# Kernel optimization log

Hardware: AMD Instinct MI355X
Metric: run time of the kernel (lower is better)

Reference implementation:

```python
import jax, jax.numpy as jnp
import numpy as np


def _ln(x, g, b, eps=1e-5):
    m = x.mean(-1, keepdims=True)
    v = ((x - m) ** 2).mean(-1, keepdims=True)
    return (x - m) * jax.lax.rsqrt(v + eps) * g + b


def setup_inputs() -> dict:
    key = jax.random.key(0)
    ks = jax.random.split(key, 12)
    B, S, I, H, E, P, O, EM = 32, 512, 64, 512, 8, 96, 64, 512
    D = S * I
    r = lambda k, shape, s=0.02: jax.random.normal(k, shape, jnp.float32) * s
    z = lambda *shape: jnp.zeros(shape, jnp.float32)
    o = lambda *shape: jnp.ones(shape, jnp.float32)
    return dict(
        x=jax.random.normal(ks[0], (B, S, I), jnp.float32),
        gW1=r(ks[1], (D, EM)), gb1=z(EM), gln1_g=o(EM), gln1_b=z(EM),
        gW2=r(ks[2], (EM, EM)), gb2=z(EM), gln2_g=o(EM), gln2_b=z(EM),
        gW3=r(ks[3], (EM, 128)), gb3=z(128),
        protos=jax.random.normal(ks[4], (E, 128), jnp.float32) * 0.01,
        temp=jnp.ones((), jnp.float32),
        eW1=r(ks[5], (E, I, H)), eb1=z(E, H),
        eW2=r(ks[6], (E, H, H)), eb2=z(E, H),
        fW1=r(ks[7], (H, H)), fb1=z(H), fln_g=o(H), fln_b=z(H),
        fW2=r(ks[8], (H, H)), fb2=z(H),
        ln_g=o(H), ln_b=z(H),
        pW1=r(ks[9], (H, H // 2)), pb1=z(H // 2), pln_g=o(H // 2), pln_b=z(H // 2),
        pW2=r(ks[10], (H // 2, P * O)), pb2=z(P * O),
        on_g=o(O), on_b=z(O),
    )


def reference(x, gW1, gb1, gln1_g, gln1_b, gW2, gb2, gln2_g, gln2_b, gW3, gb3,
              protos, temp, eW1, eb1, eW2, eb2,
              fW1, fb1, fln_g, fln_b, fW2, fb2, ln_g, ln_b,
              pW1, pb1, pln_g, pln_b, pW2, pb2, on_g, on_b):
    B, S, I = x.shape
    O = on_g.shape[0]
    P = pW2.shape[1] // O
    # 1) flow latent mapping (identity fallback path of the original code)
    x_flat = x.reshape(B, S * I)
    z_latent = x_flat
    # 2) gating encoder -> 128-d embedding (dropout = identity in eval)
    h = jax.nn.relu(_ln(z_latent @ gW1 + gb1, gln1_g, gln1_b))
    h = jax.nn.relu(_ln(h @ gW2 + gb2, gln2_g, gln2_b))
    emb = h @ gW3 + gb3  # [B, 128]
    # 3) routing: euclidean cdist to prototypes, temperature-scaled softmax
    d2 = jnp.sum((emb[:, None, :] - protos[None, :, :]) ** 2, axis=-1)
    dist = jnp.sqrt(jnp.maximum(d2, 1e-12))  # [B, E]
    t = jnp.clip(temp, 0.1, 5.0)
    w = jax.nn.softmax(-dist / t, axis=-1)  # [B, E]
    # 4) experts: per-expert FFN on raw input, all experts batched
    he = jax.nn.relu(jnp.einsum('bsi,eih->besh', x, eW1) + eb1[None, :, None, :])
    eo = jnp.einsum('besh,eho->beso', he, eW2) + eb2[None, :, None, :]  # [B,E,S,H]
    # 5) routing-weighted combine + fusion + prediction head
    fused = jnp.einsum('besh,be->bsh', eo, w)
    f = jax.nn.relu(_ln(fused @ fW1 + fb1, fln_g, fln_b)) @ fW2 + fb2
    f = _ln(f, ln_g, ln_b)
    last = f[:, -1, :]  # [B, H]
    p = jax.nn.relu(_ln(last @ pW1 + pb1, pln_g, pln_b)) @ pW2 + pb2
    p = p.reshape(B, P, O)
    return _ln(p, on_g, on_b)
```

## Files before the change

kernel.cpp:

```cpp
#include <hip/hip_runtime.h>
#include <math.h>

#define DIMK 32768

__device__ __forceinline__ void fma4(float4& a, float s, const float4 w) {
  a.x += s * w.x; a.y += s * w.y; a.z += s * w.z; a.w += s * w.w;
}

__device__ __forceinline__ float block_sum(float v, float* red, int n) {
  int t = threadIdx.x;
  red[t] = v;
  __syncthreads();
  for (int s = n >> 1; s > 0; s >>= 1) {
    if (t < s) red[t] += red[t + s];
    __syncthreads();
  }
  float r = red[0];
  __syncthreads();
  return r;
}

__global__ __launch_bounds__(256) void gemm1(const float* __restrict__ x,
                                             const float* __restrict__ gW1,
                                             float* __restrict__ part) {
  const int mt = blockIdx.x, ks = blockIdx.y;
  const int m0 = mt * 128, k0 = ks * 256;
  const int t = threadIdx.x;
  __shared__ float As[32 * 260];
  __shared__ float Ws[64 * 128];

  for (int i = t; i < 2048; i += 256) {
    int b = i >> 6, q = i & 63;
    *(float4*)&As[b * 260 + q * 4] = *(const float4*)(x + (size_t)b * DIMK + k0 + q * 4);
  }
  const float* Wp = gW1 + (size_t)k0 * 512 + m0;
  float4 wreg[8];
#pragma unroll
  for (int j = 0; j < 8; ++j) {
    int i = t + j * 256, r = i >> 5, q = i & 31;
    wreg[j] = *(const float4*)(Wp + (size_t)r * 512 + q * 4);
  }

  const int mf = t & 31, bg = t >> 5;
  const int b0 = bg * 4;
  float4 acc[4];
#pragma unroll
  for (int j = 0; j < 4; ++j) acc[j] = make_float4(0.f, 0.f, 0.f, 0.f);
  const float* a0 = &As[b0 * 260];

  for (int s = 0; s < 4; ++s) {
    __syncthreads();
#pragma unroll
    for (int j = 0; j < 8; ++j) {
      int i = t + j * 256, r = i >> 5, q = i & 31;
      *(float4*)&Ws[r * 128 + q * 4] = wreg[j];
    }
    __syncthreads();
    if (s < 3) {
      const float* Wn = Wp + (size_t)(s + 1) * 64 * 512;
#pragma unroll
      for (int j = 0; j < 8; ++j) {
        int i = t + j * 256, r = i >> 5, q = i & 31;
        wreg[j] = *(const float4*)(Wn + (size_t)r * 512 + q * 4);
      }
    }
    const float* ab = a0 + s * 64;
#pragma unroll 8
    for (int k = 0; k < 64; ++k) {
      float4 wv = *(const float4*)&Ws[k * 128 + mf * 4];
      float av0 = ab[k], av1 = ab[260 + k], av2 = ab[520 + k], av3 = ab[780 + k];
      fma4(acc[0], av0, wv);
      fma4(acc[1], av1, wv);
      fma4(acc[2], av2, wv);
      fma4(acc[3], av3, wv);
    }
  }

  float* op = part + ((size_t)ks * 32 + b0) * 512 + m0 + mf * 4;
#pragma unroll
  for (int j = 0; j < 4; ++j) *(float4*)(op + (size_t)j * 512) = acc[j];
}

__global__ __launch_bounds__(512) void gred_ln(const float* __restrict__ part,
                                               const float* __restrict__ gb1,
                                               const float* __restrict__ g, const float* __restrict__ bt,
                                               float* __restrict__ h1) {
  const int b = blockIdx.x, t = threadIdx.x;
  __shared__ float red[512];
  float a = gb1[t];
  const float* pp0 = part + (size_t)b * 512 + t;
#pragma unroll 8
  for (int ks = 0; ks < 128; ++ks) a += pp0[(size_t)ks * 16384];
  float mean = block_sum(a, red, 512) * (1.f / 512.f);
  float d = a - mean;
  float var = block_sum(d * d, red, 512) * (1.f / 512.f);
  h1[b * 512 + t] = fmaxf(d * rsqrtf(var + 1e-5f) * g[t] + bt[t], 0.f);
}

template <int KC>
__global__ __launch_bounds__(256) void gemm_tile(const float* __restrict__ A,
                                                 const float* __restrict__ W,
                                                 float* __restrict__ outp,
                                                 int M, int aRow,
                                                 size_t aStrideE, size_t wStrideE) {
  const int mt = blockIdx.x, kq = blockIdx.y, e = blockIdx.z, NE = gridDim.z;
  const int m0 = mt * 64, k0 = kq * KC;
  const int t = threadIdx.x;
  __shared__ float Ws[KC * 64];
  __shared__ float As[32 * (KC + 4)];
  const float* Wp = W + (size_t)e * wStrideE + (size_t)k0 * M + m0;
  for (int i = t; i < KC * 16; i += 256) {
    int r = i >> 4, q = i & 15;
    *(float4*)&Ws[r * 64 + q * 4] = *(const float4*)(Wp + (size_t)r * M + q * 4);
  }
  const float* Ap = A + (size_t)e * aStrideE + k0;
  for (int i = t; i < 32 * (KC / 4); i += 256) {
    int b = i / (KC / 4), q = i % (KC / 4);
    *(float4*)&As[b * (KC + 4) + q * 4] = *(const float4*)(Ap + (size_t)b * aRow + q * 4);
  }
  __syncthreads();
  const int mf = t & 15, bg = t >> 4;
  const int b0 = bg * 2;
  float4 acc0 = make_float4(0.f, 0.f, 0.f, 0.f), acc1 = acc0;
  const float* a0 = &As[b0 * (KC + 4)];
  const float* a1 = &As[(b0 + 1) * (KC + 4)];
#pragma unroll 8
  for (int k = 0; k < KC; ++k) {
    float4 wv = *(const float4*)&Ws[k * 64 + mf * 4];
    fma4(acc0, a0[k], wv);
    fma4(acc1, a1[k], wv);
  }
  float* op = outp + ((size_t)(kq * NE + e) * 32 + b0) * M + m0 + mf * 4;
  *(float4*)op = acc0;
  *(float4*)(op + M) = acc1;
}

__global__ void red_ln(const float* __restrict__ zp, const float* __restrict__ bias,
                       const float* __restrict__ g, const float* __restrict__ bt,
                       float* __restrict__ outp, int M, int nq, int relu) {
  const int b = blockIdx.x, t = threadIdx.x;
  __shared__ float red[512];
  float a = bias[t];
#pragma unroll 4
  for (int kq = 0; kq < nq; ++kq) a += zp[((size_t)kq * 32 + b) * M + t];
  float fM = 1.f / (float)M;
  float mean = block_sum(a, red, M) * fM;
  float d = a - mean;
  float var = block_sum(d * d, red, M) * fM;
  float v = d * rsqrtf(var + 1e-5f) * g[t] + bt[t];
  outp[b * M + t] = relu ? fmaxf(v, 0.f) : v;
}

__global__ __launch_bounds__(128) void gate_k(const float* __restrict__ zp2,
                                              const float* __restrict__ gb3,
                                              const float* __restrict__ protos,
                                              const float* __restrict__ temp,
                                              float* __restrict__ wgt) {
  __shared__ float red[128];
  __shared__ float d2s[8];
  const int b = blockIdx.x, t = threadIdx.x;
  float a = gb3[t];
#pragma unroll 4
  for (int kq = 0; kq < 16; ++kq) a += zp2[((size_t)kq * 32 + b) * 128 + t];
  for (int e = 0; e < 8; ++e) {
    float dd = a - protos[e * 128 + t];
    float s = block_sum(dd * dd, red, 128);
    if (t == 0) d2s[e] = s;
  }
  __syncthreads();
  if (t == 0) {
    float tt = fminf(fmaxf(temp[0], 0.1f), 5.0f);
    float lg[8], mx = -1e30f;
#pragma unroll
    for (int e = 0; e < 8; ++e) {
      float dist = sqrtf(fmaxf(d2s[e], 1e-12f));
      lg[e] = -dist / tt;
      mx = fmaxf(mx, lg[e]);
    }
    float se = 0.f;
#pragma unroll
    for (int e = 0; e < 8; ++e) { lg[e] = expf(lg[e] - mx); se += lg[e]; }
#pragma unroll
    for (int e = 0; e < 8; ++e) wgt[b * 8 + e] = lg[e] / se;
  }
}

__global__ __launch_bounds__(256) void he_k(const float* __restrict__ x,
                                            const float* __restrict__ eW1,
                                            const float* __restrict__ eb1,
                                            float* __restrict__ he_all) {
  const int e = blockIdx.x, hs = blockIdx.y;
  const int t = threadIdx.x;
  __shared__ float xs[32 * 64];
  __shared__ float Ws[64 * 256];
  for (int i = t; i < 512; i += 256) {
    int b = i >> 4, q = i & 15;
    *(float4*)&xs[b * 64 + q * 4] = *(const float4*)(x + (size_t)b * DIMK + 32704 + q * 4);
  }
  const float* w1 = eW1 + (size_t)e * 64 * 512 + hs * 256;
  for (int i = t; i < 64 * 64; i += 256) {
    int k = i >> 6, q = i & 63;
    *(float4*)&Ws[k * 256 + q * 4] = *(const float4*)(w1 + (size_t)k * 512 + q * 4);
  }
  __syncthreads();
  float acc[32];
#pragma unroll
  for (int b = 0; b < 32; ++b) acc[b] = 0.f;
#pragma unroll 4
  for (int k = 0; k < 64; ++k) {
    float wk = Ws[k * 256 + t];
#pragma unroll
    for (int b = 0; b < 32; ++b) acc[b] += xs[b * 64 + k] * wk;
  }
  float bb = eb1[e * 512 + hs * 256 + t];
  for (int b = 0; b < 32; ++b)
    he_all[((size_t)e * 32 + b) * 512 + hs * 256 + t] = fmaxf(acc[b] + bb, 0.f);
}

__global__ __launch_bounds__(512) void ffuse(const float* __restrict__ epart,
                                             const float* __restrict__ eb2,
                                             const float* __restrict__ wgt,
                                             float* __restrict__ fused) {
  const int b = blockIdx.x, t = threadIdx.x;
  __shared__ float wl[8];
  if (t < 8) wl[t] = wgt[b * 8 + t];
  __syncthreads();
  float a = 0.f;
#pragma unroll
  for (int e = 0; e < 8; ++e) {
    float s = eb2[e * 512 + t];
#pragma unroll
    for (int kq = 0; kq < 8; ++kq)
      s += epart[(((size_t)kq * 8 + e) * 32 + b) * 512 + t];
    a += wl[e] * s;
  }
  fused[b * 512 + t] = a;
}

__global__ __launch_bounds__(256) void fin_red(const float* __restrict__ fpart,
                                               const float* __restrict__ pb2,
                                               const float* __restrict__ ong,
                                               const float* __restrict__ onb,
                                               float* __restrict__ outp) {
  const int t = threadIdx.x;
  const int lane = t & 63, w = t >> 6;
  const int r = blockIdx.x * 4 + w;
  const int b = r / 96, pi = r % 96;
  const int m = pi * 64 + lane;
  float a = pb2[m];
#pragma unroll
  for (int kq = 0; kq < 8; ++kq) a += fpart[((size_t)kq * 32 + b) * 6144 + m];
  float s = a;
  s += __shfl_xor(s, 1); s += __shfl_xor(s, 2); s += __shfl_xor(s, 4);
  s += __shfl_xor(s, 8); s += __shfl_xor(s, 16); s += __shfl_xor(s, 32);
  float mean = s * (1.f / 64.f);
  float d = a - mean;
  float q = d * d;
  q += __shfl_xor(q, 1); q += __shfl_xor(q, 2); q += __shfl_xor(q, 4);
  q += __shfl_xor(q, 8); q += __shfl_xor(q, 16); q += __shfl_xor(q, 32);
  float rr = rsqrtf(q * (1.f / 64.f) + 1e-5f);
  outp[((size_t)b * 96 + pi) * 64 + lane] = d * rr * ong[lane] + onb[lane];
}

extern "C" void kernel_launch(void* const* d_in, const int* in_sizes, int n_in,
                              void* d_out, int out_size, void* d_ws, size_t ws_size,
                              hipStream_t stream) {
  (void)in_sizes; (void)n_in; (void)out_size; (void)ws_size;
  const float* x      = (const float*)d_in[0];
  const float* gW1    = (const float*)d_in[1];
  const float* gb1    = (const float*)d_in[2];
  const float* gln1_g = (const float*)d_in[3];
  const float* gln1_b = (const float*)d_in[4];
  const float* gW2    = (const float*)d_in[5];
  const float* gb2    = (const float*)d_in[6];
  const float* gln2_g = (const float*)d_in[7];
  const float* gln2_b = (const float*)d_in[8];
  const float* gW3    = (const float*)d_in[9];
  const float* gb3    = (const float*)d_in[10];
  const float* protos = (const float*)d_in[11];
  const float* temp   = (const float*)d_in[12];
  const float* eW1    = (const float*)d_in[13];
  const float* eb1    = (const float*)d_in[14];
  const float* eW2    = (const float*)d_in[15];
  const float* eb2    = (const float*)d_in[16];
  const float* fW1    = (const float*)d_in[17];
  const float* fb1    = (const float*)d_in[18];
  const float* fln_g  = (const float*)d_in[19];
  const float* fln_b  = (const float*)d_in[20];
  const float* fW2    = (const float*)d_in[21];
  const float* fb2    = (const float*)d_in[22];
  const float* ln_g   = (const float*)d_in[23];
  const float* ln_b   = (const float*)d_in[24];
  const float* pW1    = (const float*)d_in[25];
  const float* pb1    = (const float*)d_in[26];
  const float* pln_g  = (const float*)d_in[27];
  const float* pln_b  = (const float*)d_in[28];
  const float* pW2    = (const float*)d_in[29];
  const float* pb2    = (const float*)d_in[30];
  const float* on_g   = (const float*)d_in[31];
  const float* on_b   = (const float*)d_in[32];
  float* out = (float*)d_out;

  float* ws     = (float*)d_ws;
  float* part   = ws;
  float* epart  = ws;
  float* he_all = ws + 1048576;
  float* fpart  = ws;
  float* h1     = ws + 2097152;
  float* h2     = h1 + 16384;
  float* zp     = h2 + 16384;
  float* zp2    = zp + 262144;
  float* wgt    = zp2 + 65536;
  float* fused  = wgt + 256;
  float* f1     = fused + 16384;
  float* lastv  = f1 + 16384;
  float* pp     = lastv + 16384;

  gemm1<<<dim3(4, 128), 256, 0, stream>>>(x, gW1, part);
  gred_ln<<<32, 512, 0, stream>>>(part, gb1, gln1_g, gln1_b, h1);
  gemm_tile<32><<<dim3(8, 16, 1), 256, 0, stream>>>(h1, gW2, zp, 512, 512, 0, 0);
  red_ln<<<32, 512, 0, stream>>>(zp, gb2, gln2_g, gln2_b, h2, 512, 16, 1);
  gemm_tile<32><<<dim3(2, 16, 1), 256, 0, stream>>>(h2, gW3, zp2, 128, 512, 0, 0);
  gate_k<<<32, 128, 0, stream>>>(zp2, gb3, protos, temp, wgt);

  he_k<<<dim3(8, 2), 256, 0, stream>>>(x, eW1, eb1, he_all);
  gemm_tile<64><<<dim3(8, 8, 8), 256, 0, stream>>>(he_all, eW2, epart, 512, 512,
                                                   (size_t)32 * 512, (size_t)512 * 512);
  ffuse<<<32, 512, 0, stream>>>(epart, eb2, wgt, fused);

  gemm_tile<32><<<dim3(8, 16, 1), 256, 0, stream>>>(fused, fW1, zp, 512, 512, 0, 0);
  red_ln<<<32, 512, 0, stream>>>(zp, fb1, fln_g, fln_b, f1, 512, 16, 1);
  gemm_tile<32><<<dim3(8, 16, 1), 256, 0, stream>>>(f1, fW2, zp, 512, 512, 0, 0);
  red_ln<<<32, 512, 0, stream>>>(zp, fb2, ln_g, ln_b, lastv, 512, 16, 0);
  gemm_tile<32><<<dim3(4, 16, 1), 256, 0, stream>>>(lastv, pW1, zp, 256, 512, 0, 0);
  red_ln<<<32, 256, 0, stream>>>(zp, pb1, pln_g, pln_b, pp, 256, 16, 1);

  gemm_tile<32><<<dim3(96, 8, 1), 256, 0, stream>>>(pp, pW2, fpart, 6144, 256, 0, 0);
  fin_red<<<768, 256, 0, stream>>>(fpart, pb2, on_g, on_b, out);
}
```

Measured before the change: 295.3 us.

## Collapse sixteen launches into four fused kernels with per-row MLP chains

Merges the gating GEMM with the expert first layer into one grid. The gating tail (LN, GEMM2, LN, GEMM3, routing softmax) now runs alongside the expert second-layer GEMM in a single launch. The fusion and prediction chain is done per batch row inside one block, and the final projection is fused with its LayerNorm. This removes many launches and the partial-sum round trips through global memory. In exchange, the per-row blocks read full weight matrices with low parallelism (32 blocks), which may leave the GPU underused on the serial MLP chain.

```diff
diff --git a/kernel.cpp b/kernel.cpp
--- a/kernel.cpp
+++ b/kernel.cpp
@@ -7,259 +7,324 @@
   a.x += s * w.x; a.y += s * w.y; a.z += s * w.z; a.w += s * w.w;
 }
 
-__device__ __forceinline__ float block_sum(float v, float* red, int n) {
-  int t = threadIdx.x;
-  red[t] = v;
-  __syncthreads();
-  for (int s = n >> 1; s > 0; s >>= 1) {
-    if (t < s) red[t] += red[t + s];
-    __syncthreads();
-  }
-  float r = red[0];
-  __syncthreads();
-  return r;
-}
-
-__global__ __launch_bounds__(256) void gemm1(const float* __restrict__ x,
-                                             const float* __restrict__ gW1,
-                                             float* __restrict__ part) {
-  const int mt = blockIdx.x, ks = blockIdx.y;
-  const int m0 = mt * 128, k0 = ks * 256;
+__device__ __forceinline__ float bsum8(float v, volatile float* r8) {
+  for (int o = 1; o < 64; o <<= 1) v += __shfl_xor(v, o);
+  const int w = threadIdx.x >> 6;
+  __syncthreads();
+  if ((threadIdx.x & 63) == 0) r8[w] = v;
+  __syncthreads();
+  float s = 0.f;
+#pragma unroll
+  for (int i = 0; i < 8; ++i) s += r8[i];
+  return s;
+}
+
+__global__ __launch_bounds__(256) void k1_gemm1_he(const float* __restrict__ x,
+                                                   const float* __restrict__ gW1,
+                                                   const float* __restrict__ eW1,
+                                                   const float* __restrict__ eb1,
+                                                   float* __restrict__ part,
+                                                   float* __restrict__ he_all) {
+  __shared__ __align__(16) float S[18432];
   const int t = threadIdx.x;
-  __shared__ float As[32 * 260];
-  __shared__ float Ws[64 * 128];
-
-  for (int i = t; i < 2048; i += 256) {
-    int b = i >> 6, q = i & 63;
-    *(float4*)&As[b * 260 + q * 4] = *(const float4*)(x + (size_t)b * DIMK + k0 + q * 4);
-  }
-  const float* Wp = gW1 + (size_t)k0 * 512 + m0;
-  float4 wreg[8];
-#pragma unroll
-  for (int j = 0; j < 8; ++j) {
-    int i = t + j * 256, r = i >> 5, q = i & 31;
-    wreg[j] = *(const float4*)(Wp + (size_t)r * 512 + q * 4);
-  }
-
-  const int mf = t & 31, bg = t >> 5;
-  const int b0 = bg * 4;
-  float4 acc[4];
-#pragma unroll
-  for (int j = 0; j < 4; ++j) acc[j] = make_float4(0.f, 0.f, 0.f, 0.f);
-  const float* a0 = &As[b0 * 260];
-
-  for (int s = 0; s < 4; ++s) {
-    __syncthreads();
+  if (blockIdx.x < 512) {
+    const int mt = blockIdx.x & 3, ks = blockIdx.x >> 2;
+    const int m0 = mt * 128, k0 = ks * 256;
+    float* As = S;
+    float* Ws = S + 8320;
+    for (int i = t; i < 2048; i += 256) {
+      int b = i >> 6, q = i & 63;
+      *(float4*)&As[b * 260 + q * 4] = *(const float4*)(x + (size_t)b * DIMK + k0 + q * 4);
+    }
+    const float* Wp = gW1 + (size_t)k0 * 512 + m0;
+    float4 wreg[8];
 #pragma unroll
     for (int j = 0; j < 8; ++j) {
       int i = t + j * 256, r = i >> 5, q = i & 31;
-      *(float4*)&Ws[r * 128 + q * 4] = wreg[j];
-    }
-    __syncthreads();
-    if (s < 3) {
-      const float* Wn = Wp + (size_t)(s + 1) * 64 * 512;
+      wreg[j] = *(const float4*)(Wp + (size_t)r * 512 + q * 4);
+    }
+    const int mf = t & 31, bg = t >> 5;
+    const int b0 = bg * 4;
+    float4 acc[4];
+#pragma unroll
+    for (int j = 0; j < 4; ++j) acc[j] = make_float4(0.f, 0.f, 0.f, 0.f);
+    const float* a0 = &As[b0 * 260];
+    for (int s = 0; s < 4; ++s) {
+      __syncthreads();
 #pragma unroll
       for (int j = 0; j < 8; ++j) {
         int i = t + j * 256, r = i >> 5, q = i & 31;
-        wreg[j] = *(const float4*)(Wn + (size_t)r * 512 + q * 4);
-      }
-    }
-    const float* ab = a0 + s * 64;
-#pragma unroll 8
+        *(float4*)&Ws[r * 128 + q * 4] = wreg[j];
+      }
+      __syncthreads();
+      if (s < 3) {
+        const float* Wn = Wp + (size_t)(s + 1) * 64 * 512;
+#pragma unroll
+        for (int j = 0; j < 8; ++j) {
+          int i = t + j * 256, r = i >> 5, q = i & 31;
+          wreg[j] = *(const float4*)(Wn + (size_t)r * 512 + q * 4);
+        }
+      }
+      const float* ab = a0 + s * 64;
+#pragma unroll 8
+      for (int k = 0; k < 64; ++k) {
+        float4 wv = *(const float4*)&Ws[k * 128 + mf * 4];
+        fma4(acc[0], ab[k], wv);
+        fma4(acc[1], ab[260 + k], wv);
+        fma4(acc[2], ab[520 + k], wv);
+        fma4(acc[3], ab[780 + k], wv);
+      }
+    }
+    float* op = part + ((size_t)ks * 32 + b0) * 512 + m0 + mf * 4;
+#pragma unroll
+    for (int j = 0; j < 4; ++j) *(float4*)(op + (size_t)j * 512) = acc[j];
+  } else {
+    const int v = blockIdx.x - 512;
+    const int e = v >> 1, hs = v & 1;
+    float* xs = S;
+    float* Ws = S + 2048;
+    for (int i = t; i < 512; i += 256) {
+      int b = i >> 4, q = i & 15;
+      *(float4*)&xs[b * 64 + q * 4] = *(const float4*)(x + (size_t)b * DIMK + 32704 + q * 4);
+    }
+    const float* w1 = eW1 + (size_t)e * 32768 + hs * 256;
+    for (int i = t; i < 4096; i += 256) {
+      int r = i >> 6, q = i & 63;
+      *(float4*)&Ws[r * 256 + q * 4] = *(const float4*)(w1 + (size_t)r * 512 + q * 4);
+    }
+    __syncthreads();
+    float acc[32];
+#pragma unroll
+    for (int b = 0; b < 32; ++b) acc[b] = 0.f;
+#pragma unroll 4
     for (int k = 0; k < 64; ++k) {
-      float4 wv = *(const float4*)&Ws[k * 128 + mf * 4];
-      float av0 = ab[k], av1 = ab[260 + k], av2 = ab[520 + k], av3 = ab[780 + k];
-      fma4(acc[0], av0, wv);
-      fma4(acc[1], av1, wv);
-      fma4(acc[2], av2, wv);
-      fma4(acc[3], av3, wv);
-    }
-  }
-
-  float* op = part + ((size_t)ks * 32 + b0) * 512 + m0 + mf * 4;
-#pragma unroll
-  for (int j = 0; j < 4; ++j) *(float4*)(op + (size_t)j * 512) = acc[j];
-}
-
-__global__ __launch_bounds__(512) void gred_ln(const float* __restrict__ part,
-                                               const float* __restrict__ gb1,
-                                               const float* __restrict__ g, const float* __restrict__ bt,
-                                               float* __restrict__ h1) {
+      float wk = Ws[k * 256 + t];
+#pragma unroll
+      for (int b = 0; b < 32; ++b) acc[b] += xs[b * 64 + k] * wk;
+    }
+    float bb = eb1[e * 512 + hs * 256 + t];
+    for (int b = 0; b < 32; ++b)
+      he_all[((size_t)e * 32 + b) * 512 + hs * 256 + t] = fmaxf(acc[b] + bb, 0.f);
+  }
+}
+
+__global__ __launch_bounds__(512) void k2_gtail_eg(const float* __restrict__ part,
+                                                   const float* __restrict__ gb1,
+                                                   const float* __restrict__ g1g, const float* __restrict__ g1b,
+                                                   const float* __restrict__ gW2, const float* __restrict__ gb2,
+                                                   const float* __restrict__ g2g, const float* __restrict__ g2b,
+                                                   const float* __restrict__ gW3, const float* __restrict__ gb3,
+                                                   const float* __restrict__ protos, const float* __restrict__ temp,
+                                                   const float* __restrict__ he_all, const float* __restrict__ eW2,
+                                                   float* __restrict__ wgt, float* __restrict__ eo) {
+  __shared__ __align__(16) float S[16512];
+  __shared__ float hb[512], h2b[512], embp[512], embs[128], d2s[8];
+  __shared__ float r8[8];
+  const int t = threadIdx.x;
+  if (blockIdx.x < 32) {
+    const int b = blockIdx.x;
+    float a = gb1[t];
+    const float* p0 = part + (size_t)b * 512 + t;
+#pragma unroll 8
+    for (int ks = 0; ks < 128; ++ks) a += p0[(size_t)ks * 16384];
+    float mean = bsum8(a, r8) * (1.f / 512.f);
+    float d = a - mean;
+    float var = bsum8(d * d, r8) * (1.f / 512.f);
+    hb[t] = fmaxf(d * rsqrtf(var + 1e-5f) * g1g[t] + g1b[t], 0.f);
+    __syncthreads();
+    float y = gb2[t];
+    {
+      const float* wp = gW2 + t;
+#pragma unroll 8
+      for (int k = 0; k < 512; ++k) y += hb[k] * wp[(size_t)k * 512];
+    }
+    mean = bsum8(y, r8) * (1.f / 512.f);
+    d = y - mean;
+    var = bsum8(d * d, r8) * (1.f / 512.f);
+    h2b[t] = fmaxf(d * rsqrtf(var + 1e-5f) * g2g[t] + g2b[t], 0.f);
+    __syncthreads();
+    {
+      const int kh = t >> 7, m = t & 127;
+      float c = 0.f;
+      const float* w3 = gW3 + m;
+#pragma unroll 8
+      for (int k = kh * 128; k < kh * 128 + 128; ++k) c += h2b[k] * w3[(size_t)k * 128];
+      embp[t] = c;
+    }
+    __syncthreads();
+    if (t < 128) embs[t] = gb3[t] + embp[t] + embp[128 + t] + embp[256 + t] + embp[384 + t];
+    __syncthreads();
+    {
+      const int e = t >> 6, l = t & 63;
+      float z0 = embs[l] - protos[e * 128 + l];
+      float z1 = embs[l + 64] - protos[e * 128 + 64 + l];
+      float q = z0 * z0 + z1 * z1;
+      for (int o = 1; o < 64; o <<= 1) q += __shfl_xor(q, o);
+      if (l == 0) d2s[e] = q;
+    }
+    __syncthreads();
+    if (t == 0) {
+      float tt = fminf(fmaxf(temp[0], 0.1f), 5.0f);
+      float lg[8], mx = -1e30f;
+#pragma unroll
+      for (int e = 0; e < 8; ++e) {
+        float dist = sqrtf(fmaxf(d2s[e], 1e-12f));
+        lg[e] = -dist / tt;
+        mx = fmaxf(mx, lg[e]);
+      }
+      float se = 0.f;
+#pragma unroll
+      for (int e = 0; e < 8; ++e) { lg[e] = expf(lg[e] - mx); se += lg[e]; }
+#pragma unroll
+      for (int e = 0; e < 8; ++e) wgt[b * 8 + e] = lg[e] / se;
+    }
+  } else {
+    const int v = blockIdx.x - 32;
+    const int e = v >> 3, mt = v & 7;
+    const int m0 = mt * 64;
+    float* As = S;
+    float* Ws = S + 8320;
+    const int mf = t & 15, bg = t >> 4;
+    float4 acc = make_float4(0.f, 0.f, 0.f, 0.f);
+    const float* Ae = he_all + (size_t)e * 16384;
+    const float* We = eW2 + (size_t)e * 262144 + m0;
+    for (int kh = 0; kh < 2; ++kh) {
+      __syncthreads();
+      for (int i = t; i < 2048; i += 512) {
+        int b = i >> 6, q = i & 63;
+        *(float4*)&As[b * 260 + q * 4] =
+            *(const float4*)(Ae + (size_t)b * 512 + kh * 256 + q * 4);
+      }
+      for (int sub = 0; sub < 2; ++sub) {
+        __syncthreads();
+        const float* wp = We + (size_t)(kh * 256 + sub * 128) * 512;
+        for (int i = t; i < 2048; i += 512) {
+          int r = i >> 4, q = i & 15;
+          *(float4*)&Ws[r * 64 + q * 4] = *(const float4*)(wp + (size_t)r * 512 + q * 4);
+        }
+        __syncthreads();
+        const float* ar = As + bg * 260 + sub * 128;
+#pragma unroll 8
+        for (int k = 0; k < 128; ++k)
+          fma4(acc, ar[k], *(const float4*)&Ws[k * 64 + mf * 4]);
+      }
+    }
+    *(float4*)(eo + ((size_t)e * 32 + bg) * 512 + m0 + mf * 4) = acc;
+  }
+}
+
+__global__ __launch_bounds__(512) void k3_fpath(const float* __restrict__ eo,
+                                                const float* __restrict__ eb2,
+                                                const float* __restrict__ wgt,
+                                                const float* __restrict__ fW1, const float* __restrict__ fb1,
+                                                const float* __restrict__ flg, const float* __restrict__ flb,
+                                                const float* __restrict__ fW2, const float* __restrict__ fb2,
+                                                const float* __restrict__ lng, const float* __restrict__ lnb,
+                                                const float* __restrict__ pW1, const float* __restrict__ pb1,
+                                                const float* __restrict__ plg, const float* __restrict__ plb,
+                                                float* __restrict__ pp) {
+  __shared__ float rowA[512], pl[512], r8[8], wl8[8];
   const int b = blockIdx.x, t = threadIdx.x;
-  __shared__ float red[512];
-  float a = gb1[t];
-  const float* pp0 = part + (size_t)b * 512 + t;
-#pragma unroll 8
-  for (int ks = 0; ks < 128; ++ks) a += pp0[(size_t)ks * 16384];
-  float mean = block_sum(a, red, 512) * (1.f / 512.f);
-  float d = a - mean;
-  float var = block_sum(d * d, red, 512) * (1.f / 512.f);
-  h1[b * 512 + t] = fmaxf(d * rsqrtf(var + 1e-5f) * g[t] + bt[t], 0.f);
-}
-
-template <int KC>
-__global__ __launch_bounds__(256) void gemm_tile(const float* __restrict__ A,
-                                                 const float* __restrict__ W,
-                                                 float* __restrict__ outp,
-                                                 int M, int aRow,
-                                                 size_t aStrideE, size_t wStrideE) {
-  const int mt = blockIdx.x, kq = blockIdx.y, e = blockIdx.z, NE = gridDim.z;
-  const int m0 = mt * 64, k0 = kq * KC;
-  const int t = threadIdx.x;
-  __shared__ float Ws[KC * 64];
-  __shared__ float As[32 * (KC + 4)];
-  const float* Wp = W + (size_t)e * wStrideE + (size_t)k0 * M + m0;
-  for (int i = t; i < KC * 16; i += 256) {
-    int r = i >> 4, q = i & 15;
-    *(float4*)&Ws[r * 64 + q * 4] = *(const float4*)(Wp + (size_t)r * M + q * 4);
-  }
-  const float* Ap = A + (size_t)e * aStrideE + k0;
-  for (int i = t; i < 32 * (KC / 4); i += 256) {
-    int b = i / (KC / 4), q = i % (KC / 4);
-    *(float4*)&As[b * (KC + 4) + q * 4] = *(const float4*)(Ap + (size_t)b * aRow + q * 4);
-  }
-  __syncthreads();
-  const int mf = t & 15, bg = t >> 4;
-  const int b0 = bg * 2;
-  float4 acc0 = make_float4(0.f, 0.f, 0.f, 0.f), acc1 = acc0;
-  const float* a0 = &As[b0 * (KC + 4)];
-  const float* a1 = &As[(b0 + 1) * (KC + 4)];
-#pragma unroll 8
-  for (int k = 0; k < KC; ++k) {
-    float4 wv = *(const float4*)&Ws[k * 64 + mf * 4];
-    fma4(acc0, a0[k], wv);
-    fma4(acc1, a1[k], wv);
-  }
-  float* op = outp + ((size_t)(kq * NE + e) * 32 + b0) * M + m0 + mf * 4;
-  *(float4*)op = acc0;
-  *(float4*)(op + M) = acc1;
-}
-
-__global__ void red_ln(const float* __restrict__ zp, const float* __restrict__ bias,
-                       const float* __restrict__ g, const float* __restrict__ bt,
-                       float* __restrict__ outp, int M, int nq, int relu) {
-  const int b = blockIdx.x, t = threadIdx.x;
-  __shared__ float red[512];
-  float a = bias[t];
-#pragma unroll 4
-  for (int kq = 0; kq < nq; ++kq) a += zp[((size_t)kq * 32 + b) * M + t];
-  float fM = 1.f / (float)M;
-  float mean = block_sum(a, red, M) * fM;
-  float d = a - mean;
-  float var = block_sum(d * d, red, M) * fM;
-  float v = d * rsqrtf(var + 1e-5f) * g[t] + bt[t];
-  outp[b * M + t] = relu ? fmaxf(v, 0.f) : v;
-}
-
-__global__ __launch_bounds__(128) void gate_k(const float* __restrict__ zp2,
-                                              const float* __restrict__ gb3,
-                                              const float* __restrict__ protos,
-                                              const float* __restrict__ temp,
-                                              float* __restrict__ wgt) {
-  __shared__ float red[128];
-  __shared__ float d2s[8];
-  const int b = blockIdx.x, t = threadIdx.x;
-  float a = gb3[t];
-#pragma unroll 4
-  for (int kq = 0; kq < 16; ++kq) a += zp2[((size_t)kq * 32 + b) * 128 + t];
-  for (int e = 0; e < 8; ++e) {
-    float dd = a - protos[e * 128 + t];
-    float s = block_sum(dd * dd, red, 128);
-    if (t == 0) d2s[e] = s;
-  }
-  __syncthreads();
-  if (t == 0) {
-    float tt = fminf(fmaxf(temp[0], 0.1f), 5.0f);
-    float lg[8], mx = -1e30f;
-#pragma unroll
-    for (int e = 0; e < 8; ++e) {
-      float dist = sqrtf(fmaxf(d2s[e], 1e-12f));
-      lg[e] = -dist / tt;
-      mx = fmaxf(mx, lg[e]);
-    }
-    float se = 0.f;
-#pragma unroll
-    for (int e = 0; e < 8; ++e) { lg[e] = expf(lg[e] - mx); se += lg[e]; }
-#pragma unroll
-    for (int e = 0; e < 8; ++e) wgt[b * 8 + e] = lg[e] / se;
-  }
-}
-
-__global__ __launch_bounds__(256) void he_k(const float* __restrict__ x,
-                                            const float* __restrict__ eW1,
-                                            const float* __restrict__ eb1,
-                                            float* __restrict__ he_all) {
-  const int e = blockIdx.x, hs = blockIdx.y;
-  const int t = threadIdx.x;
-  __shared__ float xs[32 * 64];
-  __shared__ float Ws[64 * 256];
-  for (int i = t; i < 512; i += 256) {
-    int b = i >> 4, q = i & 15;
-    *(float4*)&xs[b * 64 + q * 4] = *(const float4*)(x + (size_t)b * DIMK + 32704 + q * 4);
-  }
-  const float* w1 = eW1 + (size_t)e * 64 * 512 + hs * 256;
-  for (int i = t; i < 64 * 64; i += 256) {
-    int k = i >> 6, q = i & 63;
-    *(float4*)&Ws[k * 256 + q * 4] = *(const float4*)(w1 + (size_t)k * 512 + q * 4);
-  }
-  __syncthreads();
-  float acc[32];
-#pragma unroll
-  for (int b = 0; b < 32; ++b) acc[b] = 0.f;
-#pragma unroll 4
-  for (int k = 0; k < 64; ++k) {
-    float wk = Ws[k * 256 + t];
-#pragma unroll
-    for (int b = 0; b < 32; ++b) acc[b] += xs[b * 64 + k] * wk;
-  }
-  float bb = eb1[e * 512 + hs * 256 + t];
-  for (int b = 0; b < 32; ++b)
-    he_all[((size_t)e * 32 + b) * 512 + hs * 256 + t] = fmaxf(acc[b] + bb, 0.f);
-}
-
-__global__ __launch_bounds__(512) void ffuse(const float* __restrict__ epart,
-                                             const float* __restrict__ eb2,
-                                             const float* __restrict__ wgt,
-                                             float* __restrict__ fused) {
-  const int b = blockIdx.x, t = threadIdx.x;
-  __shared__ float wl[8];
-  if (t < 8) wl[t] = wgt[b * 8 + t];
-  __syncthreads();
-  float a = 0.f;
-#pragma unroll
-  for (int e = 0; e < 8; ++e) {
-    float s = eb2[e * 512 + t];
-#pragma unroll
-    for (int kq = 0; kq < 8; ++kq)
-      s += epart[(((size_t)kq * 8 + e) * 32 + b) * 512 + t];
-    a += wl[e] * s;
-  }
-  fused[b * 512 + t] = a;
-}
-
-__global__ __launch_bounds__(256) void fin_red(const float* __restrict__ fpart,
+  if (t < 8) wl8[t] = wgt[b * 8 + t];
+  __syncthreads();
+  {
+    float a = 0.f;
+#pragma unroll
+    for (int e = 0; e < 8; ++e)
+      a += wl8[e] * (eo[((size_t)e * 32 + b) * 512 + t] + eb2[e * 512 + t]);
+    rowA[t] = a;
+  }
+  __syncthreads();
+  {
+    float y = fb1[t];
+    const float* wp = fW1 + t;
+#pragma unroll 8
+    for (int k = 0; k < 512; ++k) y += rowA[k] * wp[(size_t)k * 512];
+    float mean = bsum8(y, r8) * (1.f / 512.f);
+    float d = y - mean;
+    float var = bsum8(d * d, r8) * (1.f / 512.f);
+    float v = d * rsqrtf(var + 1e-5f) * flg[t] + flb[t];
+    rowA[t] = fmaxf(v, 0.f);
+  }
+  __syncthreads();
+  {
+    float y = fb2[t];
+    const float* wp = fW2 + t;
+#pragma unroll 8
+    for (int k = 0; k < 512; ++k) y += rowA[k] * wp[(size_t)k * 512];
+    float mean = bsum8(y, r8) * (1.f / 512.f);
+    float d = y - mean;
+    float var = bsum8(d * d, r8) * (1.f / 512.f);
+    rowA[t] = d * rsqrtf(var + 1e-5f) * lng[t] + lnb[t];
+  }
+  __syncthreads();
+  {
+    const int half = t >> 8, j = t & 255;
+    float c = 0.f;
+    const float* wp = pW1 + j;
+#pragma unroll 8
+    for (int k = half * 256; k < half * 256 + 256; ++k) c += rowA[k] * wp[(size_t)k * 256];
+    pl[t] = c;
+  }
+  __syncthreads();
+  float val = 0.f;
+  if (t < 256) val = pl[t] + pl[256 + t] + pb1[t];
+  float mean = bsum8(t < 256 ? val : 0.f, r8) * (1.f / 256.f);
+  float d = val - mean;
+  float var = bsum8(t < 256 ? d * d : 0.f, r8) * (1.f / 256.f);
+  if (t < 256) {
+    float v = d * rsqrtf(var + 1e-5f) * plg[t] + plb[t];
+    pp[b * 256 + t] = fmaxf(v, 0.f);
+  }
+}
+
+__global__ __launch_bounds__(256) void k4_pfin(const float* __restrict__ pp,
+                                               const float* __restrict__ pW2,
                                                const float* __restrict__ pb2,
                                                const float* __restrict__ ong,
                                                const float* __restrict__ onb,
                                                float* __restrict__ outp) {
+  __shared__ __align__(16) float Ws[256 * 64];
+  __shared__ __align__(16) float As[8 * 260];
+  const int pi = blockIdx.x, bq = blockIdx.y;
   const int t = threadIdx.x;
-  const int lane = t & 63, w = t >> 6;
-  const int r = blockIdx.x * 4 + w;
-  const int b = r / 96, pi = r % 96;
-  const int m = pi * 64 + lane;
-  float a = pb2[m];
-#pragma unroll
-  for (int kq = 0; kq < 8; ++kq) a += fpart[((size_t)kq * 32 + b) * 6144 + m];
-  float s = a;
-  s += __shfl_xor(s, 1); s += __shfl_xor(s, 2); s += __shfl_xor(s, 4);
-  s += __shfl_xor(s, 8); s += __shfl_xor(s, 16); s += __shfl_xor(s, 32);
-  float mean = s * (1.f / 64.f);
-  float d = a - mean;
-  float q = d * d;
-  q += __shfl_xor(q, 1); q += __shfl_xor(q, 2); q += __shfl_xor(q, 4);
-  q += __shfl_xor(q, 8); q += __shfl_xor(q, 16); q += __shfl_xor(q, 32);
-  float rr = rsqrtf(q * (1.f / 64.f) + 1e-5f);
-  outp[((size_t)b * 96 + pi) * 64 + lane] = d * rr * ong[lane] + onb[lane];
+  const float* wp = pW2 + pi * 64;
+  for (int i = t; i < 4096; i += 256) {
+    int r = i >> 4, q = i & 15;
+    *(float4*)&Ws[r * 64 + q * 4] = *(const float4*)(wp + (size_t)r * 6144 + q * 4);
+  }
+  for (int i = t; i < 512; i += 256) {
+    int b = i >> 6, q = i & 63;
+    *(float4*)&As[b * 260 + q * 4] = *(const float4*)(pp + (size_t)(bq * 8 + b) * 256 + q * 4);
+  }
+  __syncthreads();
+  const int w = t >> 6, o = t & 63;
+  const int bl = w * 2;
+  float a0 = 0.f, a1 = 0.f;
+  const float* ar0 = As + bl * 260;
+  const float* ar1 = ar0 + 260;
+#pragma unroll 8
+  for (int k = 0; k < 256; ++k) {
+    float wv = Ws[k * 64 + o];
+    a0 += ar0[k] * wv;
+    a1 += ar1[k] * wv;
+  }
+  float bias = pb2[pi * 64 + o];
+  float gv = ong[o], bv = onb[o];
+  float accs[2] = {a0 + bias, a1 + bias};
+#pragma unroll
+  for (int rr = 0; rr < 2; ++rr) {
+    float a = accs[rr];
+    float s = a;
+    for (int off = 1; off < 64; off <<= 1) s += __shfl_xor(s, off);
+    float mean = s * (1.f / 64.f);
+    float d = a - mean;
+    float q = d * d;
+    for (int off = 1; off < 64; off <<= 1) q += __shfl_xor(q, off);
+    float r = rsqrtf(q * (1.f / 64.f) + 1e-5f);
+    int b = bq * 8 + bl + rr;
+    outp[((size_t)b * 96 + pi) * 64 + o] = d * r * gv + bv;
+  }
 }
 
 extern "C" void kernel_launch(void* const* d_in, const int* in_sizes, int n_in,
@@ -303,38 +368,16 @@
 
   float* ws     = (float*)d_ws;
   float* part   = ws;
-  float* epart  = ws;
-  float* he_all = ws + 1048576;
-  float* fpart  = ws;
-  float* h1     = ws + 2097152;
-  float* h2     = h1 + 16384;
-  float* zp     = h2 + 16384;
-  float* zp2    = zp + 262144;
-  float* wgt    = zp2 + 65536;
-  float* fused  = wgt + 256;
-  float* f1     = fused + 16384;
-  float* lastv  = f1 + 16384;
-  float* pp     = lastv + 16384;
-
-  gemm1<<<dim3(4, 128), 256, 0, stream>>>(x, gW1, part);
-  gred_ln<<<32, 512, 0, stream>>>(part, gb1, gln1_g, gln1_b, h1);
-  gemm_tile<32><<<dim3(8, 16, 1), 256, 0, stream>>>(h1, gW2, zp, 512, 512, 0, 0);
-  red_ln<<<32, 512, 0, stream>>>(zp, gb2, gln2_g, gln2_b, h2, 512, 16, 1);
-  gemm_tile<32><<<dim3(2, 16, 1), 256, 0, stream>>>(h2, gW3, zp2, 128, 512, 0, 0);
-  gate_k<<<32, 128, 0, stream>>>(zp2, gb3, protos, temp, wgt);
-
-  he_k<<<dim3(8, 2), 256, 0, stream>>>(x, eW1, eb1, he_all);
-  gemm_tile<64><<<dim3(8, 8, 8), 256, 0, stream>>>(he_all, eW2, epart, 512, 512,
-                                                   (size_t)32 * 512, (size_t)512 * 512);
-  ffuse<<<32, 512, 0, stream>>>(epart, eb2, wgt, fused);
-
-  gemm_tile<32><<<dim3(8, 16, 1), 256, 0, stream>>>(fused, fW1, zp, 512, 512, 0, 0);
-  red_ln<<<32, 512, 0, stream>>>(zp, fb1, fln_g, fln_b, f1, 512, 16, 1);
-  gemm_tile<32><<<dim3(8, 16, 1), 256, 0, stream>>>(f1, fW2, zp, 512, 512, 0, 0);
-  red_ln<<<32, 512, 0, stream>>>(zp, fb2, ln_g, ln_b, lastv, 512, 16, 0);
-  gemm_tile<32><<<dim3(4, 16, 1), 256, 0, stream>>>(lastv, pW1, zp, 256, 512, 0, 0);
-  red_ln<<<32, 256, 0, stream>>>(zp, pb1, pln_g, pln_b, pp, 256, 16, 1);
-
-  gemm_tile<32><<<dim3(96, 8, 1), 256, 0, stream>>>(pp, pW2, fpart, 6144, 256, 0, 0);
-  fin_red<<<768, 256, 0, stream>>>(fpart, pb2, on_g, on_b, out);
-}
+  float* he_all = ws + 2097152;
+  float* eo     = ws + 2228224;
+  float* wgt    = ws + 2359296;
+  float* pp     = ws + 2359552;
+
+  k1_gemm1_he<<<528, 256, 0, stream>>>(x, gW1, eW1, eb1, part, he_all);
+  k2_gtail_eg<<<96, 512, 0, stream>>>(part, gb1, gln1_g, gln1_b, gW2, gb2,
+                                      gln2_g, gln2_b, gW3, gb3, protos, temp,
+                                      he_all, eW2, wgt, eo);
+  k3_fpath<<<32, 512, 0, stream>>>(eo, eb2, wgt, fW1, fb1, fln_g, fln_b,
+                                   fW2, fb2, ln_g, ln_b, pW1, pb1, pln_g, pln_b, pp);
+  k4_pfin<<<dim3(96, 4), 256, 0, stream>>>(pp, pW2, pb2, on_g, on_b, out);
+}
```

New measurement: 358.2 us. 21.3% more time.
